# Kernel optimization log

Measured on AMD Instinct MI355X. Metric: run time of the kernel, lower is better.

## Reference

```python
import jax, jax.numpy as jnp
import numpy as np
import math

HIDDEN = 2048
HEADS = 16
HEAD_DIM = HIDDEN // HEADS
MAX_SEQ = 4096
ROPE_BASE = 10000.0


def rope_cos_sin(seq_len):
    # (seq_len, head_dim//2) angle table
    inv_freq = 1.0 / (ROPE_BASE ** (jnp.arange(0, HEAD_DIM, 2, dtype=jnp.float32) / HEAD_DIM))
    t = jnp.arange(seq_len, dtype=jnp.float32)
    ang = jnp.einsum('s,f->sf', t, inv_freq)
    return jnp.cos(ang), jnp.sin(ang)


def apply_rope(x, cos, sin):
    # x: (b, s, h, d); interleaved complex pairs along last dim
    b, s, h, d = x.shape
    xr = x.reshape(b, s, h, d // 2, 2)
    x0, x1 = xr[..., 0], xr[..., 1]
    c = cos[:s][None, :, None, :]
    sn = sin[:s][None, :, None, :]
    o0 = x0 * c - x1 * sn
    o1 = x0 * sn + x1 * c
    return jnp.stack([o0, o1], axis=-1).reshape(b, s, h, d)


def setup_inputs() -> dict:
    key = jax.random.key(0)
    k1, k2, k3, k4, k5, k6 = jax.random.split(key, 6)
    B, SQ, SK = 2, 2048, 2048
    x = jax.random.normal(k1, (B, SQ, HIDDEN), dtype=jnp.float32)
    enc = jax.random.normal(k2, (B, SK, HIDDEN), dtype=jnp.float32)
    mask = jnp.ones((B, SK), dtype=jnp.int32)
    scale = 0.02
    Wq = jax.random.normal(k3, (HIDDEN, HIDDEN), dtype=jnp.float32) * scale
    Wk = jax.random.normal(k4, (HIDDEN, HIDDEN), dtype=jnp.float32) * scale
    Wv = jax.random.normal(k5, (HIDDEN, HIDDEN), dtype=jnp.float32) * scale
    Wo = jax.random.normal(k6, (HIDDEN, HIDDEN), dtype=jnp.float32) * scale
    return {"x": x, "encoder_output": enc, "encoder_attention_mask": mask,
            "Wq": Wq, "Wk": Wk, "Wv": Wv, "Wo": Wo}


def reference(x, encoder_output, encoder_attention_mask, Wq, Wk, Wv, Wo):
    B, SQ, _ = x.shape
    SK = encoder_output.shape[1]
    # nn.Linear(bias=False): y = x @ W^T
    q = (x @ Wq.T).reshape(B, SQ, HEADS, HEAD_DIM)
    k = (encoder_output @ Wk.T).reshape(B, SK, HEADS, HEAD_DIM)
    v = (encoder_output @ Wv.T).reshape(B, SK, HEADS, HEAD_DIM)
    cos, sin = rope_cos_sin(max(SQ, SK))
    q = apply_rope(q, cos, sin)
    k = apply_rope(k, cos, sin)
    scale = math.sqrt(HEAD_DIM)
    # (b, h, sq, sk) scores
    scores = jnp.einsum('bqhd,bkhd->bhqk', q, k) / scale
    mask = encoder_attention_mask[:, None, None, :]
    scores = jnp.where(mask == 0, -jnp.inf, scores)
    attn = jax.nn.softmax(scores, axis=-1)
    out = jnp.einsum('bhqk,bkhd->bqhd', attn, v).reshape(B, SQ, HIDDEN)
    return out @ Wo.T
```

## Files before the change

kernel.cpp:

```cpp
#include <hip/hip_runtime.h>
#include <stdint.h>


#define LOG2E 1.44269504088896340736f
#define INV2PI 0.15915494309189535f

typedef __attribute__((ext_vector_type(8))) short bf16x8;
typedef __attribute__((ext_vector_type(8))) uint16_t u16x8;
typedef __attribute__((ext_vector_type(4))) uint16_t u16x4;
typedef __attribute__((ext_vector_type(4))) float f32x4;

__device__ __forceinline__ uint16_t f2bf(float f) {
  union { float f; uint32_t i; } v; v.f = f;
  uint32_t x = v.i;
  return (uint16_t)((x + 0x7fffu + ((x >> 16) & 1u)) >> 16);
}
__device__ __forceinline__ uint32_t f_as_u(float f) { union { float f; uint32_t u; } v; v.f = f; return v.u; }
__device__ __forceinline__ float u_as_f(uint32_t u) { union { uint32_t u; float f; } v; v.u = u; return v.f; }
__device__ __forceinline__ void glds16(const void* g, void* l) {
  __builtin_amdgcn_global_load_lds((const __attribute__((address_space(1))) void*)g,
                                   (__attribute__((address_space(3))) void*)l, 16, 0, 0);
}

__global__ __launch_bounds__(256) void convert_f32_bf16(const float* __restrict__ in,
                                                        uint16_t* __restrict__ out) {
  const long i = ((long)blockIdx.x * 256 + threadIdx.x) * 8;
  const f32x4 a = *(const f32x4*)(in + i);
  const f32x4 b = *(const f32x4*)(in + i + 4);
  u16x8 o;
#pragma unroll
  for (int j = 0; j < 4; ++j) { o[j] = f2bf(a[j]); o[4 + j] = f2bf(b[j]); }
  *(u16x8*)(out + i) = o;
}

__global__ __launch_bounds__(256) void convert_w4(const float* __restrict__ Wq,
                                                  const float* __restrict__ Wk,
                                                  const float* __restrict__ Wv,
                                                  const float* __restrict__ Wo,
                                                  uint16_t* __restrict__ W4) {
  const int blk = blockIdx.x;
  const int sec = blk >> 11;
  const long off = ((long)(blk & 2047) * 256 + threadIdx.x) * 8;
  const float* src = (sec == 0) ? Wq : (sec == 1) ? Wk : (sec == 2) ? Wv : Wo;
  const f32x4 a = *(const f32x4*)(src + off);
  const f32x4 b = *(const f32x4*)(src + off + 4);
  u16x8 o;
#pragma unroll
  for (int j = 0; j < 4; ++j) { o[j] = f2bf(a[j]); o[4 + j] = f2bf(b[j]); }
  *(u16x8*)(W4 + (long)sec * 4194304 + off) = o;
}

__global__ __launch_bounds__(256) void mask_bias(const int* __restrict__ m,
                                                 float* __restrict__ bias) {
  const int i = blockIdx.x * 256 + threadIdx.x;
  bias[i] = m[i] ? 0.0f : -__builtin_inff();
}

__device__ __forceinline__ void epi_rope_store(uint16_t* C, const f32x4& a, int rowbase,
                                               int c, float oscale) {
  const int f = (c >> 1) & 63;
  const float inv = __builtin_amdgcn_exp2f((float)f * (-13.287712379549449f / 64.0f));
  const float sgn = (c & 1) ? 1.0f : -1.0f;
#pragma unroll
  for (int r = 0; r < 4; ++r) {
    const float val = a[r];
    const float partner = __shfl_xor(val, 1);
    const int s = (rowbase + r) & 2047;
    const float rev = __builtin_amdgcn_fractf((float)s * inv * INV2PI);
    const float sn = __builtin_amdgcn_sinf(rev);
    const float cs = __builtin_amdgcn_cosf(rev);
    C[(long)(rowbase + r) * 2048 + c] = f2bf((val * cs + sgn * partner * sn) * oscale);
  }
}

__global__ __launch_bounds__(512, 2) void gemm256(const uint16_t* __restrict__ A0,
                                                  const uint16_t* __restrict__ A1,
                                                  const uint16_t* __restrict__ W,
                                                  uint16_t* __restrict__ Qb,
                                                  uint16_t* __restrict__ Kb,
                                                  uint16_t* __restrict__ Vtb,
                                                  int M, int N, int K, float oscale) {
  __shared__ __align__(16) uint16_t As[2][2][8192];
  __shared__ __align__(16) uint16_t Bs[2][2][8192];
  const int tid = threadIdx.x;
  const int lane = tid & 63;
  const int w = tid >> 6;
  const int r16 = lane & 15, quad = lane >> 4;
  const int wm = w >> 2, wn = w & 3;

  const int nby = M >> 8;
  const int nwg = gridDim.x;
  const int wg = ((int)blockIdx.x & 7) * (nwg >> 3) + ((int)blockIdx.x >> 3);
  const int by = wg % nby, bx = wg / nby;
  const int m0 = by << 8, n0 = bx << 8;

  const uint16_t* A = (n0 >= 2048) ? A1 : A0;

  const int srow = 2 * w * 16 + (lane >> 2);
  const int ssl = (lane & 3) ^ ((srow >> 1) & 3);
  const uint16_t* Ag0 = A + (long)(m0 + srow) * K + ssl * 8;
  const uint16_t* Ag1 = Ag0 + (long)16 * K;
  const uint16_t* Bg0 = W + (long)(n0 + srow) * K + ssl * 8;
  const uint16_t* Bg1 = Bg0 + (long)16 * K;
  const int ldso = w << 10;

  const int sw = (r16 >> 1) & 3;
  const int aoff = (wm * 128 + r16) * 32 + ((quad ^ sw) << 3);
  const int boff = (wn * 64 + r16) * 32 + ((quad ^ sw) << 3);

  f32x4 acc[8][4] = {};
  bf16x8 af[4], bfr[4];

#define SCHED0() __builtin_amdgcn_sched_barrier(0)
#define G_STAGE_A(BUF, KK, T) do { \
    glds16(Ag0 + (long)(T) * 64 + (KK) * 32, &As[BUF][KK][ldso]); \
    glds16(Ag1 + (long)(T) * 64 + (KK) * 32, &As[BUF][KK][ldso + 512]); } while (0)
#define G_STAGE_B(BUF, KK, T) do { \
    glds16(Bg0 + (long)(T) * 64 + (KK) * 32, &Bs[BUF][KK][ldso]); \
    glds16(Bg1 + (long)(T) * 64 + (KK) * 32, &Bs[BUF][KK][ldso + 512]); } while (0)
#define LDS_B(BUF, KK) do { _Pragma("unroll") \
    for (int i = 0; i < 4; ++i) bfr[i] = *(const bf16x8*)&Bs[BUF][KK][boff + i * 512]; } while (0)
#define LDS_A(BUF, KK, MH) do { _Pragma("unroll") \
    for (int i = 0; i < 4; ++i) af[i] = *(const bf16x8*)&As[BUF][KK][aoff + ((MH) * 4 + i) * 512]; } while (0)
#define MFMA16(MH) do { __builtin_amdgcn_s_setprio(1); _Pragma("unroll") \
    for (int mi = 0; mi < 4; ++mi) { _Pragma("unroll") \
      for (int nt = 0; nt < 4; ++nt) \
        acc[(MH) * 4 + mi][nt] = __builtin_amdgcn_mfma_f32_16x16x32_bf16(af[mi], bfr[nt], acc[(MH) * 4 + mi][nt], 0, 0, 0); } \
    __builtin_amdgcn_s_setprio(0); } while (0)
#define VMBAR(NN) do { SCHED0(); \
    asm volatile("s_waitcnt vmcnt(" #NN ")" ::: "memory"); \
    __builtin_amdgcn_s_barrier(); \
    SCHED0(); } while (0)
#define TILE_ITER(T, BC, BN) do { \
    G_STAGE_A(BN, 0, (T) + 1); LDS_B(BC, 0); LDS_A(BC, 0, 0); MFMA16(0); \
    G_STAGE_B(BN, 0, (T) + 1); LDS_A(BC, 0, 1); MFMA16(1); \
    VMBAR(4); \
    G_STAGE_A(BN, 1, (T) + 1); LDS_B(BC, 1); LDS_A(BC, 1, 0); MFMA16(0); \
    G_STAGE_B(BN, 1, (T) + 1); LDS_A(BC, 1, 1); MFMA16(1); \
    VMBAR(4); } while (0)

  G_STAGE_A(0, 0, 0); G_STAGE_B(0, 0, 0); G_STAGE_A(0, 1, 0); G_STAGE_B(0, 1, 0);
  VMBAR(4);

  const int NT = K >> 6;
  int t = 0;
  for (; t + 2 < NT; t += 2) { TILE_ITER(t, 0, 1); TILE_ITER(t + 1, 1, 0); }
  TILE_ITER(t, 0, 1);

  LDS_B(1, 0); LDS_A(1, 0, 0); MFMA16(0);
  LDS_A(1, 0, 1); MFMA16(1);
  VMBAR(0);
  LDS_B(1, 1); LDS_A(1, 1, 0); MFMA16(0);
  LDS_A(1, 1, 1); MFMA16(1);

#undef G_STAGE_A
#undef G_STAGE_B
#undef LDS_A
#undef LDS_B
#undef TILE_ITER

#pragma unroll
  for (int mt = 0; mt < 8; ++mt)
#pragma unroll
    for (int nt = 0; nt < 4; ++nt) {
      const int col = n0 + wn * 64 + nt * 16 + r16;
      const int rowbase = m0 + wm * 128 + mt * 16 + quad * 4;
      if (n0 < 2048) {
        epi_rope_store(Qb, acc[mt][nt], rowbase, col, oscale);
      } else if (n0 < 4096) {
        epi_rope_store(Kb, acc[mt][nt], rowbase, col - 2048, 1.0f);
      } else {
        const int c = col - 4096;
        const int h = c >> 7, d = c & 127;
        const int b = rowbase >> 11, s = rowbase & 2047;
        u16x4 pk;
#pragma unroll
        for (int r = 0; r < 4; ++r) pk[r] = f2bf(acc[mt][nt][r]);
        *(u16x4*)(Vtb + (long)((b * 16 + h) * 128 + d) * 2048 + s) = pk;
      }
    }
}

__global__ __launch_bounds__(512, 2) void gemm_proj(const uint16_t* __restrict__ A0,
                                                    const uint16_t* __restrict__ W,
                                                    float* __restrict__ C,
                                                    int M, int N, int K) {
  __shared__ __align__(16) uint16_t As[2][2][4096];
  __shared__ __align__(16) uint16_t Bs[2][2][8192];
  const int tid = threadIdx.x;
  const int lane = tid & 63;
  const int w = tid >> 6;
  const int r16 = lane & 15, quad = lane >> 4;
  const int wm = w >> 2, wn = w & 3;

  const int nby = M >> 7;
  const int nwg = gridDim.x;
  const int wg = ((int)blockIdx.x & 7) * (nwg >> 3) + ((int)blockIdx.x >> 3);
  const int by = wg % nby, bx = wg / nby;
  const int m0 = by << 7, n0 = bx << 8;

  const int sa_row = 16 * w + (lane >> 2);
  const int sb_row = 32 * w + (lane >> 2);
  const int ssl = (lane & 3) ^ (((lane >> 2) >> 1) & 3);
  const uint16_t* Ag = A0 + (long)(m0 + sa_row) * K + ssl * 8;
  const uint16_t* Bg0 = W + (long)(n0 + sb_row) * K + ssl * 8;
  const uint16_t* Bg1 = Bg0 + (long)16 * K;

  const int sw = (r16 >> 1) & 3;
  const int aoff = (wm * 64 + r16) * 32 + ((quad ^ sw) << 3);
  const int boff = (wn * 64 + r16) * 32 + ((quad ^ sw) << 3);

  f32x4 acc[4][4] = {};
  bf16x8 af[4], bfr[4];

#define PG_STAGE_A(BUF, KK, T) \
    glds16(Ag + (long)(T) * 64 + (KK) * 32, &As[BUF][KK][w * 512])
#define PG_STAGE_B(BUF, KK, T) do { \
    glds16(Bg0 + (long)(T) * 64 + (KK) * 32, &Bs[BUF][KK][2 * w * 512]); \
    glds16(Bg1 + (long)(T) * 64 + (KK) * 32, &Bs[BUF][KK][2 * w * 512 + 512]); } while (0)
#define PLDS_B(BUF, KK) do { _Pragma("unroll") \
    for (int i = 0; i < 4; ++i) bfr[i] = *(const bf16x8*)&Bs[BUF][KK][boff + i * 512]; } while (0)
#define PLDS_A(BUF, KK) do { _Pragma("unroll") \
    for (int i = 0; i < 4; ++i) af[i] = *(const bf16x8*)&As[BUF][KK][aoff + i * 512]; } while (0)
#define PMFMA(MT0, MT1) do { __builtin_amdgcn_s_setprio(1); _Pragma("unroll") \
    for (int mi = (MT0); mi < (MT1); ++mi) { _Pragma("unroll") \
      for (int nt = 0; nt < 4; ++nt) \
        acc[mi][nt] = __builtin_amdgcn_mfma_f32_16x16x32_bf16(af[mi], bfr[nt], acc[mi][nt], 0, 0, 0); } \
    __builtin_amdgcn_s_setprio(0); } while (0)
#define PTILE(T, BC, BN) do { \
    PG_STAGE_A(BN, 0, (T) + 1); PLDS_B(BC, 0); PLDS_A(BC, 0); PMFMA(0, 2); \
    PG_STAGE_B(BN, 0, (T) + 1); PMFMA(2, 4); \
    VMBAR(3); \
    PG_STAGE_A(BN, 1, (T) + 1); PLDS_B(BC, 1); PLDS_A(BC, 1); PMFMA(0, 2); \
    PG_STAGE_B(BN, 1, (T) + 1); PMFMA(2, 4); \
    VMBAR(3); } while (0)

  PG_STAGE_A(0, 0, 0); PG_STAGE_B(0, 0, 0); PG_STAGE_A(0, 1, 0); PG_STAGE_B(0, 1, 0);
  VMBAR(3);

  const int NT = K >> 6;
  int t = 0;
  for (; t + 2 < NT; t += 2) { PTILE(t, 0, 1); PTILE(t + 1, 1, 0); }
  PTILE(t, 0, 1);

  PLDS_B(1, 0); PLDS_A(1, 0); PMFMA(0, 4);
  VMBAR(0);
  PLDS_B(1, 1); PLDS_A(1, 1); PMFMA(0, 4);

#undef PG_STAGE_A
#undef PG_STAGE_B
#undef PLDS_A
#undef PLDS_B
#undef PMFMA
#undef PTILE
#undef MFMA16
#undef VMBAR
#undef SCHED0

#pragma unroll
  for (int mt = 0; mt < 4; ++mt)
#pragma unroll
    for (int nt = 0; nt < 4; ++nt) {
      const int col = n0 + wn * 64 + nt * 16 + r16;
      const int rowbase = m0 + wm * 64 + mt * 16 + quad * 4;
#pragma unroll
      for (int r = 0; r < 4; ++r)
        C[(long)(rowbase + r) * N + col] = acc[mt][nt][r];
    }
}

__global__ __launch_bounds__(512, 4) void attn_kernel(const uint16_t* __restrict__ Q,
                                                      const uint16_t* __restrict__ K,
                                                      const uint16_t* __restrict__ Vt,
                                                      const float* __restrict__ bias,
                                                      uint16_t* __restrict__ O) {
  __shared__ __align__(16) uint16_t Ks[2][32 * 128];
  __shared__ __align__(16) uint16_t Vts[2][128 * 32];
  __shared__ __align__(16) uint16_t Ps[8][16 * 40];
  const int tid = threadIdx.x;
  const int lane = tid & 63;
  const int w = tid >> 6;
  const int r16 = lane & 15, quad = lane >> 4;
  const int h = blockIdx.y, b = blockIdx.z;
  const int qbase = blockIdx.x * 128 + w * 16;

  bf16x8 qf[4];
  {
    const uint16_t* qb = Q + ((long)(b * 2048 + qbase + r16)) * 2048 + h * 128 + quad * 8;
#pragma unroll
    for (int c = 0; c < 4; ++c) qf[c] = *(const bf16x8*)(qb + c * 32);
  }
  f32x4 oacc[8] = {};
  float li[4] = {};

  uint16_t* PsW = &Ps[w][0];
  const float* brow = bias + b * 2048;

  const int kkey = 4 * w + quad;
  const uint16_t* kg = K + ((long)(b * 2048 + kkey)) * 2048 + h * 128
                         + 8 * (r16 ^ (kkey & 7));
  const int vdim = 16 * w + (lane >> 2);
  const uint16_t* vg = Vt + ((long)((b * 16 + h) * 128 + vdim)) * 2048
                          + 8 * ((lane & 3) ^ ((lane >> 2) & 3));

  glds16(kg, &Ks[0][w * 512]);
  glds16(vg, &Vts[0][w * 512]);
  kg += 32 * 2048;
  vg += 32;
  float bn0 = brow[r16], bn1 = brow[16 + r16];

  auto body = [&](int k0, const uint16_t* Kc, const uint16_t* Vc,
                  uint16_t* Kn, uint16_t* Vn, bool pf) {
    __syncthreads();
    const float bc0 = bn0, bc1 = bn1;
    if (pf) {
      glds16(kg, Kn + w * 512);
      glds16(vg, Vn + w * 512);
      kg += 32 * 2048;
      vg += 32;
      bn0 = brow[k0 + 32 + r16];
      bn1 = brow[k0 + 48 + r16];
    }
#pragma unroll
    for (int ct = 0; ct < 2; ++ct) {
      const int key = ct * 16 + r16;
      const int kb = key & 7;
      bf16x8 kf[4];
#pragma unroll
      for (int c = 0; c < 4; ++c)
        kf[c] = *(const bf16x8*)(Kc + key * 128 + ((4 * c + quad) ^ kb) * 8);
      const float bv = ct ? bc1 : bc0;
      const int pc = ct * 2 + (r16 >> 3);
      f32x4 s = {};
#pragma unroll
      for (int c = 0; c < 4; ++c)
        s = __builtin_amdgcn_mfma_f32_16x16x32_bf16(qf[c], kf[c], s, 0, 0, 0);
#pragma unroll
      for (int r = 0; r < 4; ++r) {
        const float p = __builtin_amdgcn_exp2f(s[r] + bv);
        const uint32_t pb = f_as_u(p) + 0x8000u;
        const int row = quad * 4 + r;
        PsW[row * 40 + ((pc ^ quad) << 3) + (r16 & 7)] = (uint16_t)(pb >> 16);
        li[r] += u_as_f(pb & 0xffff0000u);
      }
    }
    bf16x8 pa = *(const bf16x8*)(PsW + r16 * 40 + ((quad ^ (r16 >> 2)) << 3));
#pragma unroll
    for (int nt = 0; nt < 8; ++nt) {
      const int dim = nt * 16 + r16;
      bf16x8 vf = *(const bf16x8*)(Vc + dim * 32 + ((quad ^ (dim & 3)) << 3));
      oacc[nt] = __builtin_amdgcn_mfma_f32_16x16x32_bf16(pa, vf, oacc[nt], 0, 0, 0);
    }
  };

  for (int kt2 = 0; kt2 < 32; ++kt2) {
    body(64 * kt2,      &Ks[0][0], &Vts[0][0], &Ks[1][0], &Vts[1][0], true);
    body(64 * kt2 + 32, &Ks[1][0], &Vts[1][0], &Ks[0][0], &Vts[0][0], kt2 < 31);
  }

#pragma unroll
  for (int off = 1; off < 16; off <<= 1)
#pragma unroll
    for (int r = 0; r < 4; ++r) li[r] += __shfl_xor(li[r], off);

  uint16_t* ob = O + ((long)(b * 2048 + qbase)) * 2048 + h * 128;
  float inv_l[4];
#pragma unroll
  for (int r = 0; r < 4; ++r) inv_l[r] = 1.0f / li[r];
#pragma unroll
  for (int nt = 0; nt < 8; ++nt)
#pragma unroll
    for (int r = 0; r < 4; ++r)
      ob[(long)(quad * 4 + r) * 2048 + nt * 16 + r16] = f2bf(oacc[nt][r] * inv_l[r]);
}

extern "C" void kernel_launch(void* const* d_in, const int* in_sizes, int n_in,
                              void* d_out, int out_size, void* d_ws, size_t ws_size,
                              hipStream_t stream) {
  const float* x   = (const float*)d_in[0];
  const float* enc = (const float*)d_in[1];
  const int*   msk = (const int*)d_in[2];
  const float* Wq  = (const float*)d_in[3];
  const float* Wk  = (const float*)d_in[4];
  const float* Wv  = (const float*)d_in[5];
  const float* Wo  = (const float*)d_in[6];
  float* out = (float*)d_out;

  const long NELT = 8L * 1024 * 1024;
  const long WELT = 4L * 1024 * 1024;
  uint16_t* Qb  = (uint16_t*)d_ws;
  uint16_t* Kb  = Qb + NELT;
  uint16_t* Vtb = Kb + NELT;
  uint16_t* W4  = Vtb + NELT;
  float* biasb  = (float*)(W4 + 4 * WELT);
  uint16_t* xb   = (uint16_t*)d_out;
  uint16_t* encb = xb + NELT;
  uint16_t* Ob   = W4;

  const float cs_exp = 0.088388347648318447f * LOG2E;

  convert_f32_bf16<<<(int)(NELT / 2048), 256, 0, stream>>>(x, xb);
  convert_f32_bf16<<<(int)(NELT / 2048), 256, 0, stream>>>(enc, encb);
  convert_w4<<<8192, 256, 0, stream>>>(Wq, Wk, Wv, Wo, W4);
  mask_bias<<<16, 256, 0, stream>>>(msk, biasb);

  gemm256<<<384, 512, 0, stream>>>(xb, encb, W4, Qb, Kb, Vtb,
                                   4096, 6144, 2048, cs_exp);

  attn_kernel<<<dim3(16, 16, 2), 512, 0, stream>>>(Qb, Kb, Vtb, biasb, Ob);

  gemm_proj<<<256, 512, 0, stream>>>(Ob, W4 + 3 * WELT, out, 4096, 2048, 2048);
}
```

Before: 445.3 us.

## Halve gemm256 LDS buffers and simplify pipeline to raise occupancy

```diff
diff --git a/kernel.cpp b/kernel.cpp
--- a/kernel.cpp
+++ b/kernel.cpp
@@ -73,15 +73,15 @@
   }
 }
 
-__global__ __launch_bounds__(512, 2) void gemm256(const uint16_t* __restrict__ A0,
+__global__ __launch_bounds__(512, 4) void gemm256(const uint16_t* __restrict__ A0,
                                                   const uint16_t* __restrict__ A1,
                                                   const uint16_t* __restrict__ W,
                                                   uint16_t* __restrict__ Qb,
                                                   uint16_t* __restrict__ Kb,
                                                   uint16_t* __restrict__ Vtb,
                                                   int M, int N, int K, float oscale) {
-  __shared__ __align__(16) uint16_t As[2][2][8192];
-  __shared__ __align__(16) uint16_t Bs[2][2][8192];
+  __shared__ __align__(16) uint16_t As[2][8192];
+  __shared__ __align__(16) uint16_t Bs[2][8192];
   const int tid = threadIdx.x;
   const int lane = tid & 63;
   const int w = tid >> 6;
@@ -111,53 +111,38 @@
   f32x4 acc[8][4] = {};
   bf16x8 af[4], bfr[4];
 
-#define SCHED0() __builtin_amdgcn_sched_barrier(0)
-#define G_STAGE_A(BUF, KK, T) do { \
-    glds16(Ag0 + (long)(T) * 64 + (KK) * 32, &As[BUF][KK][ldso]); \
-    glds16(Ag1 + (long)(T) * 64 + (KK) * 32, &As[BUF][KK][ldso + 512]); } while (0)
-#define G_STAGE_B(BUF, KK, T) do { \
-    glds16(Bg0 + (long)(T) * 64 + (KK) * 32, &Bs[BUF][KK][ldso]); \
-    glds16(Bg1 + (long)(T) * 64 + (KK) * 32, &Bs[BUF][KK][ldso + 512]); } while (0)
-#define LDS_B(BUF, KK) do { _Pragma("unroll") \
-    for (int i = 0; i < 4; ++i) bfr[i] = *(const bf16x8*)&Bs[BUF][KK][boff + i * 512]; } while (0)
-#define LDS_A(BUF, KK, MH) do { _Pragma("unroll") \
-    for (int i = 0; i < 4; ++i) af[i] = *(const bf16x8*)&As[BUF][KK][aoff + ((MH) * 4 + i) * 512]; } while (0)
+#define G_STAGE(BUF, C) do { \
+    glds16(Ag0 + (long)(C) * 32, &As[BUF][ldso]); \
+    glds16(Ag1 + (long)(C) * 32, &As[BUF][ldso + 512]); \
+    glds16(Bg0 + (long)(C) * 32, &Bs[BUF][ldso]); \
+    glds16(Bg1 + (long)(C) * 32, &Bs[BUF][ldso + 512]); } while (0)
+#define LDS_B(BUF) do { _Pragma("unroll") \
+    for (int i = 0; i < 4; ++i) bfr[i] = *(const bf16x8*)&Bs[BUF][boff + i * 512]; } while (0)
+#define LDS_A(BUF, MH) do { _Pragma("unroll") \
+    for (int i = 0; i < 4; ++i) af[i] = *(const bf16x8*)&As[BUF][aoff + ((MH) * 4 + i) * 512]; } while (0)
 #define MFMA16(MH) do { __builtin_amdgcn_s_setprio(1); _Pragma("unroll") \
     for (int mi = 0; mi < 4; ++mi) { _Pragma("unroll") \
       for (int nt = 0; nt < 4; ++nt) \
         acc[(MH) * 4 + mi][nt] = __builtin_amdgcn_mfma_f32_16x16x32_bf16(af[mi], bfr[nt], acc[(MH) * 4 + mi][nt], 0, 0, 0); } \
     __builtin_amdgcn_s_setprio(0); } while (0)
-#define VMBAR(NN) do { SCHED0(); \
-    asm volatile("s_waitcnt vmcnt(" #NN ")" ::: "memory"); \
-    __builtin_amdgcn_s_barrier(); \
-    SCHED0(); } while (0)
-#define TILE_ITER(T, BC, BN) do { \
-    G_STAGE_A(BN, 0, (T) + 1); LDS_B(BC, 0); LDS_A(BC, 0, 0); MFMA16(0); \
-    G_STAGE_B(BN, 0, (T) + 1); LDS_A(BC, 0, 1); MFMA16(1); \
-    VMBAR(4); \
-    G_STAGE_A(BN, 1, (T) + 1); LDS_B(BC, 1); LDS_A(BC, 1, 0); MFMA16(0); \
-    G_STAGE_B(BN, 1, (T) + 1); LDS_A(BC, 1, 1); MFMA16(1); \
-    VMBAR(4); } while (0)
-
-  G_STAGE_A(0, 0, 0); G_STAGE_B(0, 0, 0); G_STAGE_A(0, 1, 0); G_STAGE_B(0, 1, 0);
-  VMBAR(4);
-
-  const int NT = K >> 6;
-  int t = 0;
-  for (; t + 2 < NT; t += 2) { TILE_ITER(t, 0, 1); TILE_ITER(t + 1, 1, 0); }
-  TILE_ITER(t, 0, 1);
-
-  LDS_B(1, 0); LDS_A(1, 0, 0); MFMA16(0);
-  LDS_A(1, 0, 1); MFMA16(1);
-  VMBAR(0);
-  LDS_B(1, 1); LDS_A(1, 1, 0); MFMA16(0);
-  LDS_A(1, 1, 1); MFMA16(1);
-
-#undef G_STAGE_A
-#undef G_STAGE_B
+
+  G_STAGE(0, 0);
+  __syncthreads();
+
+  const int NC = K >> 5;
+  for (int c = 0; c < NC; ++c) {
+    const int cur = c & 1;
+    if (c + 1 < NC) G_STAGE(cur ^ 1, c + 1);
+    LDS_B(cur);
+    LDS_A(cur, 0); MFMA16(0);
+    LDS_A(cur, 1); MFMA16(1);
+    __syncthreads();
+  }
+
+#undef G_STAGE
 #undef LDS_A
 #undef LDS_B
-#undef TILE_ITER
+#undef MFMA16
 
 #pragma unroll
   for (int mt = 0; mt < 8; ++mt)
@@ -213,6 +198,11 @@
   f32x4 acc[4][4] = {};
   bf16x8 af[4], bfr[4];
 
+#define SCHED0() __builtin_amdgcn_sched_barrier(0)
+#define VMBAR(NN) do { SCHED0(); \
+    asm volatile("s_waitcnt vmcnt(" #NN ")" ::: "memory"); \
+    __builtin_amdgcn_s_barrier(); \
+    SCHED0(); } while (0)
 #define PG_STAGE_A(BUF, KK, T) \
     glds16(Ag + (long)(T) * 64 + (KK) * 32, &As[BUF][KK][w * 512])
 #define PG_STAGE_B(BUF, KK, T) do { \
@@ -253,7 +243,6 @@
 #undef PLDS_B
 #undef PMFMA
 #undef PTILE
-#undef MFMA16
 #undef VMBAR
 #undef SCHED0
 
```

Measured after the change: 1.319 ms. +196.1%, slower.
